# Kernel optimization log

Measured on AMD Instinct MI355X. Metric: run time of the kernel, lower is better.

The kernel has to match this reference:

```python
import jax, jax.numpy as jnp
import numpy as np

H = 1024          # hiddenSize
V = 50257         # outputSize (vocab)
L = 512           # maxLength (encoder length)


def setup_inputs() -> dict:
    key = jax.random.key(0)
    ks = jax.random.split(key, 16)
    s = 0.02
    return {
        "input": jax.random.randint(ks[0], (1,), 0, V),
        "hidden": jax.random.normal(ks[1], (1, 1, H), jnp.float32),
        "encoder_outputs": jax.random.normal(ks[2], (L, H), jnp.float32),
        "emb": jax.random.normal(ks[3], (V, H), jnp.float32) * s,
        "W_attn": jax.random.normal(ks[4], (L, 2 * H), jnp.float32) * s,
        "b_attn": jnp.zeros((L,), jnp.float32),
        "W_comb": jax.random.normal(ks[5], (H, 2 * H), jnp.float32) * s,
        "b_comb": jnp.zeros((H,), jnp.float32),
        "W_ih": jax.random.normal(ks[6], (3 * H, H), jnp.float32) * s,
        "W_hh": jax.random.normal(ks[7], (3 * H, H), jnp.float32) * s,
        "b_ih": jnp.zeros((3 * H,), jnp.float32),
        "b_hh": jnp.zeros((3 * H,), jnp.float32),
        "W_out": jax.random.normal(ks[8], (V, H), jnp.float32) * s,
        "b_out": jnp.zeros((V,), jnp.float32),
    }


def reference(input, hidden, encoder_outputs, emb, W_attn, b_attn,
              W_comb, b_comb, W_ih, W_hh, b_ih, b_hh, W_out, b_out):
    # embedding lookup: [1, H] (dropout p=0 -> identity)
    embedded = emb[input]
    h = hidden[0]                                   # [1, H]
    # attention over encoder positions
    attn_logits = jnp.concatenate([embedded, h], axis=1) @ W_attn.T + b_attn
    attn_weights = jax.nn.softmax(attn_logits, axis=1)      # [1, L]
    attn_applied = attn_weights @ encoder_outputs           # [1, H]
    # combine and relu
    x = jnp.concatenate([embedded, attn_applied], axis=1) @ W_comb.T + b_comb
    x = jax.nn.relu(x)                                      # [1, H]
    # single GRU step (PyTorch gate layout: r, z, n)
    gi = x @ W_ih.T + b_ih                                  # [1, 3H]
    gh = h @ W_hh.T + b_hh                                  # [1, 3H]
    i_r, i_z, i_n = jnp.split(gi, 3, axis=1)
    h_r, h_z, h_n = jnp.split(gh, 3, axis=1)
    r = jax.nn.sigmoid(i_r + h_r)
    z = jax.nn.sigmoid(i_z + h_z)
    n = jnp.tanh(i_n + r * h_n)
    h_new = (1.0 - z) * n + z * h                           # [1, H]
    # output distribution
    output = jax.nn.log_softmax(h_new @ W_out.T + b_out, axis=1)  # [1, V]
    return output, h_new[None], attn_weights
```

## Files before the change

### kernel.cpp

```cpp
#include <hip/hip_runtime.h>
#include <cmath>

#define H 1024
#define V 50257
#define L 512

__device__ __forceinline__ float wred_sum(float v) {
#pragma unroll
    for (int o = 32; o > 0; o >>= 1) v += __shfl_xor(v, o, 64);
    return v;
}
__device__ __forceinline__ float wred_max(float v) {
#pragma unroll
    for (int o = 32; o > 0; o >>= 1) v = fmaxf(v, __shfl_xor(v, o, 64));
    return v;
}
__device__ __forceinline__ float dot4(float4 a, float4 b) {
    return a.x * b.x + a.y * b.y + a.z * b.z + a.w * b.w;
}

__global__ void k_attn_logits(const int* __restrict__ tok,
                              const float* __restrict__ hid,
                              const float* __restrict__ emb,
                              const float* __restrict__ Wa,
                              const float* __restrict__ ba,
                              float* __restrict__ lg) {
    const int l = blockIdx.x;
    const int t = threadIdx.x;
    const float4* wr = (const float4*)(Wa + (size_t)l * 2048);
    const float4* e4 = (const float4*)(emb + (size_t)tok[0] * H);
    const float4* h4 = (const float4*)hid;
    float acc = 0.f;
#pragma unroll
    for (int i = 0; i < 2; ++i) {
        int f = t + i * 256;
        float4 w = wr[f];
        float4 s = (f < 256) ? e4[f] : h4[f - 256];
        acc += dot4(w, s);
    }
    __shared__ float sm[4];
    int lane = t & 63, wv = t >> 6;
    acc = wred_sum(acc);
    if (lane == 0) sm[wv] = acc;
    __syncthreads();
    if (t == 0) lg[l] = sm[0] + sm[1] + sm[2] + sm[3] + ba[l];
}

__global__ void k_softmax(const float* __restrict__ lg,
                          float* __restrict__ wout,
                          float* __restrict__ aa) {
    const int t = threadIdx.x;
    const int lane = t & 63, wv = t >> 6;
    __shared__ float sm[8];
    __shared__ float bc;
    float v = lg[t];
    float m = wred_max(v);
    if (lane == 0) sm[wv] = m;
    __syncthreads();
    if (t == 0) {
        float M = sm[0];
#pragma unroll
        for (int i = 1; i < 8; ++i) M = fmaxf(M, sm[i]);
        bc = M;
    }
    __syncthreads();
    const float M = bc;
    float e = expf(v - M);
    float s = wred_sum(e);
    __syncthreads();
    if (lane == 0) sm[wv] = s;
    __syncthreads();
    if (t == 0) {
        float S = 0.f;
#pragma unroll
        for (int i = 0; i < 8; ++i) S += sm[i];
        bc = S;
    }
    __syncthreads();
    wout[t] = e / bc;
    aa[t] = 0.f;
    aa[t + 512] = 0.f;
}

__global__ void k_attn_apply(const float* __restrict__ w,
                             const float* __restrict__ enc,
                             float* __restrict__ aa) {
    const int c = blockIdx.x * 256 + threadIdx.x;
    const int l0 = blockIdx.y * 32;
    float acc = 0.f;
#pragma unroll 8
    for (int l = l0; l < l0 + 32; ++l) acc += w[l] * enc[(size_t)l * H + c];
    atomicAdd(&aa[c], acc);
}

__global__ void k_comb(const int* __restrict__ tok,
                       const float* __restrict__ emb,
                       const float* __restrict__ aa,
                       const float* __restrict__ Wc,
                       const float* __restrict__ bc_,
                       float* __restrict__ xv) {
    const int j = blockIdx.x;
    const int t = threadIdx.x;
    const float4* wr = (const float4*)(Wc + (size_t)j * 2048);
    const float4* e4 = (const float4*)(emb + (size_t)tok[0] * H);
    const float4* a4 = (const float4*)aa;
    float acc = 0.f;
#pragma unroll
    for (int i = 0; i < 2; ++i) {
        int f = t + i * 256;
        float4 w = wr[f];
        float4 s = (f < 256) ? e4[f] : a4[f - 256];
        acc += dot4(w, s);
    }
    __shared__ float sm[4];
    int lane = t & 63, wv = t >> 6;
    acc = wred_sum(acc);
    if (lane == 0) sm[wv] = acc;
    __syncthreads();
    if (t == 0) xv[j] = fmaxf(sm[0] + sm[1] + sm[2] + sm[3] + bc_[j], 0.f);
}

__global__ void k_gates(const float* __restrict__ xv,
                        const float* __restrict__ hid,
                        const float* __restrict__ Wih,
                        const float* __restrict__ Whh,
                        const float* __restrict__ bih,
                        const float* __restrict__ bhh,
                        float* __restrict__ gi,
                        float* __restrict__ gh) {
    const int j = blockIdx.x;
    const int t = threadIdx.x;
    const float4* wi = (const float4*)(Wih + (size_t)j * H);
    const float4* wh = (const float4*)(Whh + (size_t)j * H);
    const float4* x4 = (const float4*)xv;
    const float4* h4 = (const float4*)hid;
    float a1 = dot4(wi[t], x4[t]);
    float a2 = dot4(wh[t], h4[t]);
    __shared__ float smA[4], smB[4];
    int lane = t & 63, wv = t >> 6;
    a1 = wred_sum(a1);
    a2 = wred_sum(a2);
    if (lane == 0) { smA[wv] = a1; smB[wv] = a2; }
    __syncthreads();
    if (t == 0) {
        gi[j] = smA[0] + smA[1] + smA[2] + smA[3] + bih[j];
        gh[j] = smB[0] + smB[1] + smB[2] + smB[3] + bhh[j];
    }
}

__global__ void k_gru(const float* __restrict__ gi,
                      const float* __restrict__ gh,
                      const float* __restrict__ hid,
                      float* __restrict__ hnew_out,
                      float* __restrict__ hnew_ws) {
    const int j = blockIdx.x * 256 + threadIdx.x;
    float r = 1.f / (1.f + expf(-(gi[j] + gh[j])));
    float z = 1.f / (1.f + expf(-(gi[H + j] + gh[H + j])));
    float n = tanhf(gi[2 * H + j] + r * gh[2 * H + j]);
    float hn = (1.f - z) * n + z * hid[j];
    hnew_out[j] = hn;
    hnew_ws[j] = hn;
}

__global__ void k_out_gemv(const float* __restrict__ hn,
                           const float* __restrict__ Wo,
                           const float* __restrict__ bo,
                           float* __restrict__ logits) {
    const int lane = threadIdx.x & 63, wv = threadIdx.x >> 6;
    const int v = blockIdx.x * 4 + wv;
    if (v >= V) return;
    const float4* wr = (const float4*)(Wo + (size_t)v * H);
    const float4* h4 = (const float4*)hn;
    float acc = 0.f;
#pragma unroll
    for (int i = 0; i < 4; ++i) {
        int f = i * 64 + lane;
        acc += dot4(wr[f], h4[f]);
    }
    acc = wred_sum(acc);
    if (lane == 0) logits[v] = acc + bo[v];
}

__global__ void k_pmax(const float* __restrict__ logits,
                       float* __restrict__ pmax,
                       float* __restrict__ S) {
    const int CH = (V + 63) / 64;
    const int b = blockIdx.x, t = threadIdx.x;
    const int s = b * CH, e = min(s + CH, V);
    float m = -INFINITY;
    for (int i = s + t; i < e; i += 256) m = fmaxf(m, logits[i]);
    __shared__ float sm[4];
    int lane = t & 63, wv = t >> 6;
    m = wred_max(m);
    if (lane == 0) sm[wv] = m;
    __syncthreads();
    if (t == 0) {
        pmax[b] = fmaxf(fmaxf(sm[0], sm[1]), fmaxf(sm[2], sm[3]));
        if (b == 0) S[0] = 0.f;
    }
}

__global__ void k_expsum(const float* __restrict__ logits,
                         const float* __restrict__ pmax,
                         float* __restrict__ S,
                         float* __restrict__ Mout) {
    float M = -INFINITY;
#pragma unroll
    for (int i = 0; i < 64; ++i) M = fmaxf(M, pmax[i]);
    const int CH = (V + 63) / 64;
    const int b = blockIdx.x, t = threadIdx.x;
    const int s = b * CH, e = min(s + CH, V);
    float acc = 0.f;
    for (int i = s + t; i < e; i += 256) acc += expf(logits[i] - M);
    __shared__ float sm[4];
    int lane = t & 63, wv = t >> 6;
    acc = wred_sum(acc);
    if (lane == 0) sm[wv] = acc;
    __syncthreads();
    if (t == 0) {
        atomicAdd(S, sm[0] + sm[1] + sm[2] + sm[3]);
        if (b == 0) Mout[0] = M;
    }
}

__global__ void k_logsm(float* __restrict__ out,
                        const float* __restrict__ S,
                        const float* __restrict__ M) {
    const int v = blockIdx.x * 256 + threadIdx.x;
    if (v < V) out[v] = out[v] - M[0] - logf(S[0]);
}

extern "C" void kernel_launch(void* const* d_in, const int* in_sizes, int n_in,
                              void* d_out, int out_size, void* d_ws, size_t ws_size,
                              hipStream_t stream) {
    const int*   tok = (const int*)d_in[0];
    const float* hid = (const float*)d_in[1];
    const float* enc = (const float*)d_in[2];
    const float* emb = (const float*)d_in[3];
    const float* Wa  = (const float*)d_in[4];
    const float* ba  = (const float*)d_in[5];
    const float* Wc  = (const float*)d_in[6];
    const float* bc  = (const float*)d_in[7];
    const float* Wih = (const float*)d_in[8];
    const float* Whh = (const float*)d_in[9];
    const float* bih = (const float*)d_in[10];
    const float* bhh = (const float*)d_in[11];
    const float* Wo  = (const float*)d_in[12];
    const float* bo  = (const float*)d_in[13];

    float* out = (float*)d_out;
    float* ws  = (float*)d_ws;
    float* wlog = ws;
    float* aa   = ws + 512;
    float* xv   = ws + 1536;
    float* gi   = ws + 2560;
    float* gh   = ws + 5632;
    float* hn   = ws + 8704;
    float* pmax = ws + 9728;
    float* S    = ws + 9792;
    float* M    = ws + 9796;

    float* out_logits = out;
    float* out_hnew   = out + V;
    float* out_attnw  = out + V + H;

    k_attn_logits<<<L, 256, 0, stream>>>(tok, hid, emb, Wa, ba, wlog);
    k_softmax<<<1, 512, 0, stream>>>(wlog, out_attnw, aa);
    k_attn_apply<<<dim3(4, 16), 256, 0, stream>>>(out_attnw, enc, aa);
    k_comb<<<H, 256, 0, stream>>>(tok, emb, aa, Wc, bc, xv);
    k_gates<<<3 * H, 256, 0, stream>>>(xv, hid, Wih, Whh, bih, bhh, gi, gh);
    k_gru<<<4, 256, 0, stream>>>(gi, gh, hid, out_hnew, hn);
    k_out_gemv<<<(V + 3) / 4, 256, 0, stream>>>(hn, Wo, bo, out_logits);
    k_pmax<<<64, 256, 0, stream>>>(out_logits, pmax, S);
    k_expsum<<<64, 256, 0, stream>>>(out_logits, pmax, S, M);
    k_logsm<<<(V + 255) / 256, 256, 0, stream>>>(out_logits, S, M);
}
```

Before: 63.38 us.

## Fuse decoder step into six kernels with online softmax in output GEMV

```diff
diff --git a/kernel.cpp b/kernel.cpp
--- a/kernel.cpp
+++ b/kernel.cpp
@@ -4,6 +4,7 @@
 #define H 1024
 #define V 50257
 #define L 512
+#define NB5 1571
 
 __device__ __forceinline__ float wred_sum(float v) {
 #pragma unroll
@@ -18,216 +19,222 @@
 __device__ __forceinline__ float dot4(float4 a, float4 b) {
     return a.x * b.x + a.y * b.y + a.z * b.z + a.w * b.w;
 }
-
-__global__ void k_attn_logits(const int* __restrict__ tok,
-                              const float* __restrict__ hid,
-                              const float* __restrict__ emb,
-                              const float* __restrict__ Wa,
-                              const float* __restrict__ ba,
-                              float* __restrict__ lg) {
-    const int l = blockIdx.x;
-    const int t = threadIdx.x;
-    const float4* wr = (const float4*)(Wa + (size_t)l * 2048);
-    const float4* e4 = (const float4*)(emb + (size_t)tok[0] * H);
-    const float4* h4 = (const float4*)hid;
-    float acc = 0.f;
-#pragma unroll
-    for (int i = 0; i < 2; ++i) {
-        int f = t + i * 256;
-        float4 w = wr[f];
-        float4 s = (f < 256) ? e4[f] : h4[f - 256];
-        acc += dot4(w, s);
-    }
-    __shared__ float sm[4];
-    int lane = t & 63, wv = t >> 6;
-    acc = wred_sum(acc);
-    if (lane == 0) sm[wv] = acc;
-    __syncthreads();
-    if (t == 0) lg[l] = sm[0] + sm[1] + sm[2] + sm[3] + ba[l];
-}
-
-__global__ void k_softmax(const float* __restrict__ lg,
-                          float* __restrict__ wout,
-                          float* __restrict__ aa) {
+__device__ __forceinline__ void ms_merge(float& m, float& s, float m2, float s2) {
+    float M = fmaxf(m, m2);
+    if (M == -INFINITY) { m = M; s = 0.f; return; }
+    s = s * expf(m - M) + s2 * expf(m2 - M);
+    m = M;
+}
+
+__global__ void k_phase1(const int* __restrict__ tok,
+                         const float* __restrict__ hid,
+                         const float* __restrict__ emb,
+                         const float* __restrict__ Wa,
+                         const float* __restrict__ ba,
+                         const float* __restrict__ Whh,
+                         const float* __restrict__ bhh,
+                         float* __restrict__ lg,
+                         float* __restrict__ gh,
+                         float* __restrict__ aa) {
     const int t = threadIdx.x;
     const int lane = t & 63, wv = t >> 6;
-    __shared__ float sm[8];
-    __shared__ float bc;
-    float v = lg[t];
-    float m = wred_max(v);
-    if (lane == 0) sm[wv] = m;
-    __syncthreads();
-    if (t == 0) {
-        float M = sm[0];
-#pragma unroll
-        for (int i = 1; i < 8; ++i) M = fmaxf(M, sm[i]);
-        bc = M;
-    }
-    __syncthreads();
-    const float M = bc;
-    float e = expf(v - M);
-    float s = wred_sum(e);
-    __syncthreads();
-    if (lane == 0) sm[wv] = s;
-    __syncthreads();
-    if (t == 0) {
-        float S = 0.f;
-#pragma unroll
-        for (int i = 0; i < 8; ++i) S += sm[i];
-        bc = S;
-    }
-    __syncthreads();
-    wout[t] = e / bc;
-    aa[t] = 0.f;
-    aa[t + 512] = 0.f;
-}
-
-__global__ void k_attn_apply(const float* __restrict__ w,
-                             const float* __restrict__ enc,
-                             float* __restrict__ aa) {
-    const int c = blockIdx.x * 256 + threadIdx.x;
-    const int l0 = blockIdx.y * 32;
-    float acc = 0.f;
-#pragma unroll 8
-    for (int l = l0; l < l0 + 32; ++l) acc += w[l] * enc[(size_t)l * H + c];
-    atomicAdd(&aa[c], acc);
+    if (blockIdx.x < 512) {
+        const int l = blockIdx.x;
+        const float4* wr = (const float4*)(Wa + (size_t)l * 2048);
+        const float4* e4 = (const float4*)(emb + (size_t)tok[0] * H);
+        const float4* h4 = (const float4*)hid;
+        float acc = 0.f;
+#pragma unroll
+        for (int i = 0; i < 2; ++i) {
+            int f = t + i * 256;
+            float4 w = wr[f];
+            float4 s = (f < 256) ? e4[f] : h4[f - 256];
+            acc += dot4(w, s);
+        }
+        __shared__ float sm[4];
+        acc = wred_sum(acc);
+        if (lane == 0) sm[wv] = acc;
+        __syncthreads();
+        if (t == 0) lg[l] = sm[0] + sm[1] + sm[2] + sm[3] + ba[l];
+    } else {
+        const int j = (blockIdx.x - 512) * 4 + wv;
+        const float4* wh = (const float4*)(Whh + (size_t)j * H);
+        const float4* h4 = (const float4*)hid;
+        float acc = 0.f;
+#pragma unroll
+        for (int k = 0; k < 4; ++k) {
+            int f = 64 * k + lane;
+            acc += dot4(wh[f], h4[f]);
+        }
+        acc = wred_sum(acc);
+        if (lane == 0) gh[j] = acc + bhh[j];
+        if (blockIdx.x == 512) {
+            aa[t] = 0.f; aa[t + 256] = 0.f; aa[t + 512] = 0.f; aa[t + 768] = 0.f;
+        }
+    }
+}
+
+__global__ void k_attn(const float* __restrict__ lg,
+                       const float* __restrict__ enc,
+                       float* __restrict__ wout,
+                       float* __restrict__ aa) {
+    const int t = threadIdx.x;
+    const int lane = t & 63, wv = t >> 6;
+    __shared__ float red[4];
+    __shared__ float swL[512];
+    float v0 = lg[t], v1 = lg[t + 256];
+    float m = wred_max(fmaxf(v0, v1));
+    if (lane == 0) red[wv] = m;
+    __syncthreads();
+    const float M = fmaxf(fmaxf(red[0], red[1]), fmaxf(red[2], red[3]));
+    float e0 = expf(v0 - M), e1 = expf(v1 - M);
+    float sl = wred_sum(e0 + e1);
+    __syncthreads();
+    if (lane == 0) red[wv] = sl;
+    __syncthreads();
+    const float S = red[0] + red[1] + red[2] + red[3];
+    swL[t] = e0 / S;
+    swL[t + 256] = e1 / S;
+    __syncthreads();
+    if (blockIdx.x == 0) { wout[t] = swL[t]; wout[t + 256] = swL[t + 256]; }
+    const int l0 = blockIdx.x * 16;
+    float a0 = 0.f, a1 = 0.f, a2 = 0.f, a3 = 0.f;
+#pragma unroll 4
+    for (int l = l0; l < l0 + 16; ++l) {
+        const float w = swL[l];
+        const float* er = enc + (size_t)l * H;
+        a0 += w * er[t];
+        a1 += w * er[t + 256];
+        a2 += w * er[t + 512];
+        a3 += w * er[t + 768];
+    }
+    atomicAdd(&aa[t], a0);
+    atomicAdd(&aa[t + 256], a1);
+    atomicAdd(&aa[t + 512], a2);
+    atomicAdd(&aa[t + 768], a3);
 }
 
 __global__ void k_comb(const int* __restrict__ tok,
                        const float* __restrict__ emb,
                        const float* __restrict__ aa,
                        const float* __restrict__ Wc,
-                       const float* __restrict__ bc_,
+                       const float* __restrict__ bcb,
                        float* __restrict__ xv) {
-    const int j = blockIdx.x;
-    const int t = threadIdx.x;
+    const int lane = threadIdx.x & 63, wv = threadIdx.x >> 6;
+    const int j = blockIdx.x * 4 + wv;
     const float4* wr = (const float4*)(Wc + (size_t)j * 2048);
     const float4* e4 = (const float4*)(emb + (size_t)tok[0] * H);
     const float4* a4 = (const float4*)aa;
     float acc = 0.f;
 #pragma unroll
-    for (int i = 0; i < 2; ++i) {
-        int f = t + i * 256;
-        float4 w = wr[f];
-        float4 s = (f < 256) ? e4[f] : a4[f - 256];
-        acc += dot4(w, s);
-    }
-    __shared__ float sm[4];
-    int lane = t & 63, wv = t >> 6;
+    for (int k = 0; k < 8; ++k) {
+        int f = 64 * k + lane;
+        float4 s = (k < 4) ? e4[f] : a4[f - 256];
+        acc += dot4(wr[f], s);
+    }
     acc = wred_sum(acc);
-    if (lane == 0) sm[wv] = acc;
-    __syncthreads();
-    if (t == 0) xv[j] = fmaxf(sm[0] + sm[1] + sm[2] + sm[3] + bc_[j], 0.f);
-}
-
-__global__ void k_gates(const float* __restrict__ xv,
-                        const float* __restrict__ hid,
-                        const float* __restrict__ Wih,
-                        const float* __restrict__ Whh,
-                        const float* __restrict__ bih,
-                        const float* __restrict__ bhh,
-                        float* __restrict__ gi,
-                        float* __restrict__ gh) {
-    const int j = blockIdx.x;
-    const int t = threadIdx.x;
-    const float4* wi = (const float4*)(Wih + (size_t)j * H);
-    const float4* wh = (const float4*)(Whh + (size_t)j * H);
+    if (lane == 0) xv[j] = fmaxf(acc + bcb[j], 0.f);
+}
+
+__global__ void k_gates_gru(const float* __restrict__ xv,
+                            const float* __restrict__ hid,
+                            const float* __restrict__ Wih,
+                            const float* __restrict__ bih,
+                            const float* __restrict__ gh,
+                            float* __restrict__ hn_out,
+                            float* __restrict__ hn_ws) {
+    const int lane = threadIdx.x & 63, wv = threadIdx.x >> 6;
+    const int j = blockIdx.x * 4 + wv;
     const float4* x4 = (const float4*)xv;
-    const float4* h4 = (const float4*)hid;
-    float a1 = dot4(wi[t], x4[t]);
-    float a2 = dot4(wh[t], h4[t]);
-    __shared__ float smA[4], smB[4];
-    int lane = t & 63, wv = t >> 6;
-    a1 = wred_sum(a1);
-    a2 = wred_sum(a2);
-    if (lane == 0) { smA[wv] = a1; smB[wv] = a2; }
-    __syncthreads();
-    if (t == 0) {
-        gi[j] = smA[0] + smA[1] + smA[2] + smA[3] + bih[j];
-        gh[j] = smB[0] + smB[1] + smB[2] + smB[3] + bhh[j];
-    }
-}
-
-__global__ void k_gru(const float* __restrict__ gi,
-                      const float* __restrict__ gh,
-                      const float* __restrict__ hid,
-                      float* __restrict__ hnew_out,
-                      float* __restrict__ hnew_ws) {
-    const int j = blockIdx.x * 256 + threadIdx.x;
-    float r = 1.f / (1.f + expf(-(gi[j] + gh[j])));
-    float z = 1.f / (1.f + expf(-(gi[H + j] + gh[H + j])));
-    float n = tanhf(gi[2 * H + j] + r * gh[2 * H + j]);
-    float hn = (1.f - z) * n + z * hid[j];
-    hnew_out[j] = hn;
-    hnew_ws[j] = hn;
+    float4 xreg[4];
+#pragma unroll
+    for (int k = 0; k < 4; ++k) xreg[k] = x4[64 * k + lane];
+    float g[3];
+#pragma unroll
+    for (int p = 0; p < 3; ++p) {
+        const float4* wr = (const float4*)(Wih + (size_t)(j + p * H) * H);
+        float acc = 0.f;
+#pragma unroll
+        for (int k = 0; k < 4; ++k) acc += dot4(wr[64 * k + lane], xreg[k]);
+        g[p] = wred_sum(acc) + bih[j + p * H];
+    }
+    if (lane == 0) {
+        float r = 1.f / (1.f + expf(-(g[0] + gh[j])));
+        float z = 1.f / (1.f + expf(-(g[1] + gh[j + H])));
+        float n = tanhf(g[2] + r * gh[j + 2 * H]);
+        float hv = (1.f - z) * n + z * hid[j];
+        hn_out[j] = hv;
+        hn_ws[j] = hv;
+    }
 }
 
 __global__ void k_out_gemv(const float* __restrict__ hn,
                            const float* __restrict__ Wo,
                            const float* __restrict__ bo,
-                           float* __restrict__ logits) {
+                           float* __restrict__ logits,
+                           float* __restrict__ pm,
+                           float* __restrict__ ps) {
     const int lane = threadIdx.x & 63, wv = threadIdx.x >> 6;
-    const int v = blockIdx.x * 4 + wv;
-    if (v >= V) return;
-    const float4* wr = (const float4*)(Wo + (size_t)v * H);
+    const int b = blockIdx.x;
     const float4* h4 = (const float4*)hn;
-    float acc = 0.f;
-#pragma unroll
-    for (int i = 0; i < 4; ++i) {
-        int f = i * 64 + lane;
-        acc += dot4(wr[f], h4[f]);
-    }
-    acc = wred_sum(acc);
-    if (lane == 0) logits[v] = acc + bo[v];
-}
-
-__global__ void k_pmax(const float* __restrict__ logits,
-                       float* __restrict__ pmax,
-                       float* __restrict__ S) {
-    const int CH = (V + 63) / 64;
-    const int b = blockIdx.x, t = threadIdx.x;
-    const int s = b * CH, e = min(s + CH, V);
-    float m = -INFINITY;
-    for (int i = s + t; i < e; i += 256) m = fmaxf(m, logits[i]);
-    __shared__ float sm[4];
-    int lane = t & 63, wv = t >> 6;
-    m = wred_max(m);
-    if (lane == 0) sm[wv] = m;
+    float4 hreg[4];
+#pragma unroll
+    for (int k = 0; k < 4; ++k) hreg[k] = h4[64 * k + lane];
+    float m = -INFINITY, s = 0.f;
+#pragma unroll
+    for (int i = 0; i < 8; ++i) {
+        const int v = b * 32 + wv * 8 + i;
+        if (v < V) {
+            const float4* wr = (const float4*)(Wo + (size_t)v * H);
+            float acc = 0.f;
+#pragma unroll
+            for (int k = 0; k < 4; ++k) acc += dot4(wr[64 * k + lane], hreg[k]);
+            acc = wred_sum(acc);
+            const float logit = acc + bo[v];
+            if (lane == 0) logits[v] = logit;
+            const float M = fmaxf(m, logit);
+            s = s * expf(m - M) + expf(logit - M);
+            m = M;
+        }
+    }
+    __shared__ float smm[4], sms[4];
+    if (lane == 0) { smm[wv] = m; sms[wv] = s; }
+    __syncthreads();
+    if (threadIdx.x == 0) {
+        float M = smm[0], S = sms[0];
+#pragma unroll
+        for (int i = 1; i < 4; ++i) ms_merge(M, S, smm[i], sms[i]);
+        pm[b] = M; ps[b] = S;
+    }
+}
+
+__global__ void k_finalize(float* __restrict__ out,
+                           const float* __restrict__ pm,
+                           const float* __restrict__ ps) {
+    const int t = threadIdx.x;
+    const int lane = t & 63, wv = t >> 6;
+    float m = -INFINITY, s = 0.f;
+    for (int i = t; i < NB5; i += 256) ms_merge(m, s, pm[i], ps[i]);
+#pragma unroll
+    for (int o = 32; o > 0; o >>= 1) {
+        float m2 = __shfl_xor(m, o, 64);
+        float s2 = __shfl_xor(s, o, 64);
+        ms_merge(m, s, m2, s2);
+    }
+    __shared__ float smm[4], sms[4];
+    __shared__ float Cs;
+    if (lane == 0) { smm[wv] = m; sms[wv] = s; }
     __syncthreads();
     if (t == 0) {
-        pmax[b] = fmaxf(fmaxf(sm[0], sm[1]), fmaxf(sm[2], sm[3]));
-        if (b == 0) S[0] = 0.f;
-    }
-}
-
-__global__ void k_expsum(const float* __restrict__ logits,
-                         const float* __restrict__ pmax,
-                         float* __restrict__ S,
-                         float* __restrict__ Mout) {
-    float M = -INFINITY;
-#pragma unroll
-    for (int i = 0; i < 64; ++i) M = fmaxf(M, pmax[i]);
-    const int CH = (V + 63) / 64;
-    const int b = blockIdx.x, t = threadIdx.x;
-    const int s = b * CH, e = min(s + CH, V);
-    float acc = 0.f;
-    for (int i = s + t; i < e; i += 256) acc += expf(logits[i] - M);
-    __shared__ float sm[4];
-    int lane = t & 63, wv = t >> 6;
-    acc = wred_sum(acc);
-    if (lane == 0) sm[wv] = acc;
-    __syncthreads();
-    if (t == 0) {
-        atomicAdd(S, sm[0] + sm[1] + sm[2] + sm[3]);
-        if (b == 0) Mout[0] = M;
-    }
-}
-
-__global__ void k_logsm(float* __restrict__ out,
-                        const float* __restrict__ S,
-                        const float* __restrict__ M) {
-    const int v = blockIdx.x * 256 + threadIdx.x;
-    if (v < V) out[v] = out[v] - M[0] - logf(S[0]);
+        float M = smm[0], S = sms[0];
+#pragma unroll
+        for (int i = 1; i < 4; ++i) ms_merge(M, S, smm[i], sms[i]);
+        Cs = M + logf(S);
+    }
+    __syncthreads();
+    const float C = Cs;
+    const int v = blockIdx.x * 256 + t;
+    if (v < V) out[v] -= C;
 }
 
 extern "C" void kernel_launch(void* const* d_in, const int* in_sizes, int n_in,
@@ -253,25 +260,19 @@
     float* wlog = ws;
     float* aa   = ws + 512;
     float* xv   = ws + 1536;
-    float* gi   = ws + 2560;
-    float* gh   = ws + 5632;
-    float* hn   = ws + 8704;
-    float* pmax = ws + 9728;
-    float* S    = ws + 9792;
-    float* M    = ws + 9796;
+    float* gh   = ws + 2560;
+    float* hn   = ws + 5632;
+    float* pm   = ws + 6656;
+    float* psum = ws + 8256;
 
     float* out_logits = out;
     float* out_hnew   = out + V;
     float* out_attnw  = out + V + H;
 
-    k_attn_logits<<<L, 256, 0, stream>>>(tok, hid, emb, Wa, ba, wlog);
-    k_softmax<<<1, 512, 0, stream>>>(wlog, out_attnw, aa);
-    k_attn_apply<<<dim3(4, 16), 256, 0, stream>>>(out_attnw, enc, aa);
-    k_comb<<<H, 256, 0, stream>>>(tok, emb, aa, Wc, bc, xv);
-    k_gates<<<3 * H, 256, 0, stream>>>(xv, hid, Wih, Whh, bih, bhh, gi, gh);
-    k_gru<<<4, 256, 0, stream>>>(gi, gh, hid, out_hnew, hn);
-    k_out_gemv<<<(V + 3) / 4, 256, 0, stream>>>(hn, Wo, bo, out_logits);
-    k_pmax<<<64, 256, 0, stream>>>(out_logits, pmax, S);
-    k_expsum<<<64, 256, 0, stream>>>(out_logits, pmax, S, M);
-    k_logsm<<<(V + 255) / 256, 256, 0, stream>>>(out_logits, S, M);
-}
+    k_phase1<<<1280, 256, 0, stream>>>(tok, hid, emb, Wa, ba, Whh, bhh, wlog, gh, aa);
+    k_attn<<<32, 256, 0, stream>>>(wlog, enc, out_attnw, aa);
+    k_comb<<<256, 256, 0, stream>>>(tok, emb, aa, Wc, bc, xv);
+    k_gates_gru<<<256, 256, 0, stream>>>(xv, hid, Wih, bih, gh, out_hnew, hn);
+    k_out_gemv<<<NB5, 256, 0, stream>>>(hn, Wo, bo, out_logits, pm, psum);
+    k_finalize<<<197, 256, 0, stream>>>(out_logits, pm, psum);
+}
```

Result: faster. 58.45 us (-7.8%).
